# Kernel tuning notes

Hardware: AMD Instinct MI355X
Metric: run time of the kernel (lower is better)

Reference implementation:

```python
import jax, jax.numpy as jnp
import numpy as np


def setup_inputs() -> dict:
    key = jax.random.key(0)
    ks = jax.random.split(key, 11)
    B, S, D, H, O = 128, 512, 256, 512, 256
    sc = lambda fan_in: 1.0 / np.sqrt(fan_in)
    return {
        "inputs": jax.random.normal(ks[0], (B, S, D), dtype=jnp.float32),
        "time_diffs": jax.random.uniform(ks[1], (B, S), dtype=jnp.float32),
        "seq_lens": jax.random.randint(ks[2], (B,), 1, S, dtype=jnp.int32),
        "W_all": jax.random.normal(ks[3], (D, 4 * H), dtype=jnp.float32) * sc(D),
        "b_all": jax.random.normal(ks[4], (4 * H,), dtype=jnp.float32) * sc(D),
        "U_all": jax.random.normal(ks[5], (H, 4 * H), dtype=jnp.float32) * sc(H),
        "b_u": jax.random.normal(ks[6], (4 * H,), dtype=jnp.float32) * sc(H),
        "W_d": jax.random.normal(ks[7], (H, H), dtype=jnp.float32) * sc(H),
        "b_d": jax.random.normal(ks[8], (H,), dtype=jnp.float32) * sc(H),
        "W_out": jax.random.normal(ks[9], (H, O), dtype=jnp.float32) * sc(H),
        "b_out": jax.random.normal(ks[10], (O,), dtype=jnp.float32) * sc(H),
    }


def reference(inputs, time_diffs, seq_lens, W_all, b_all, U_all, b_u, W_d, b_d, W_out, b_out):
    B, S, D = inputs.shape
    H = W_d.shape[0]
    # Precompute input projection for all timesteps as one batched GEMM: [B,S,4H]
    Wx = jnp.einsum("bsd,dh->bsh", inputs, W_all) + b_all

    def step(carry, xs):
        h, c = carry
        wx, t = xs  # wx: [B,4H], t: [B]
        # time-decay adjustment of cell state
        c_st = jax.nn.sigmoid(c @ W_d + b_d)
        c_adj = c - c_st + c_st * t[:, None]
        outs = wx + h @ U_all + b_u
        f, i, o, g = jnp.split(outs, 4, axis=1)
        c_t = jax.nn.sigmoid(f) * c_adj + jax.nn.sigmoid(i) * jnp.tanh(g)
        h_t = jax.nn.sigmoid(o) * jnp.tanh(c_t)
        return (h_t, c_t), (h_t, c_t)

    h0 = jnp.zeros((B, H), dtype=inputs.dtype)
    c0 = jnp.zeros((B, H), dtype=inputs.dtype)
    # scan over time (leading axis)
    xs = (jnp.swapaxes(Wx, 0, 1), time_diffs.T)  # [S,B,4H], [S,B]
    _, (hs, cs) = jax.lax.scan(step, (h0, c0), xs)
    hs = jnp.swapaxes(hs, 0, 1)  # [B,S,H]
    cs = jnp.swapaxes(cs, 0, 1)
    outputs = jnp.einsum("bsh,ho->bso", hs, W_out) + b_out
    return outputs, hs, cs
```

## Files before the change

### kernel.cpp

```cpp
#include <hip/hip_runtime.h>

typedef __attribute__((ext_vector_type(8))) short short8;
typedef __attribute__((ext_vector_type(4))) float floatx4;
typedef unsigned short u16;
typedef __attribute__((ext_vector_type(4))) unsigned short u16x4;

#define B_ 128
#define S_ 512
#define D_ 256
#define H_ 512
#define O_ 256

__device__ __forceinline__ u16 f2bf(float f) {
  union { float f; unsigned u; } v; v.f = f;
  unsigned r = v.u + 0x7fffu + ((v.u >> 16) & 1u);
  return (u16)(r >> 16);
}
__device__ __forceinline__ float sigf(float x) { return 1.f / (1.f + __expf(-x)); }
__device__ __forceinline__ float tanhf_fast(float x) { return 1.f - 2.f / (__expf(2.f * x) + 1.f); }

__device__ __forceinline__ unsigned long long ld_u64_agent(const unsigned long long* p) {
  return __hip_atomic_load(p, __ATOMIC_RELAXED, __HIP_MEMORY_SCOPE_AGENT);
}

__global__ __launch_bounds__(256) void cvt_bf16_vec(const float* __restrict__ in,
                                                    u16* __restrict__ out, int n4) {
  int i = blockIdx.x * 256 + threadIdx.x;
  if (i < n4) {
    const float4 v = ((const float4*)in)[i];
    u16x4 o;
    o.x = f2bf(v.x); o.y = f2bf(v.y); o.z = f2bf(v.z); o.w = f2bf(v.w);
    ((u16x4*)out)[i] = o;
  }
}

__global__ __launch_bounds__(256) void transpose_cvt(const float* __restrict__ in,
                                                     u16* __restrict__ out, int R, int C) {
  int idx = blockIdx.x * 256 + threadIdx.x;
  if (idx < R * C) {
    int r = idx % R, c = idx / R;
    out[idx] = f2bf(in[(size_t)r * C + c]);
  }
}

#define PU 520
#define PX 264
#define SCAN_SMEM ((size_t)(4*16*PU + 4*16*PX + 3*16*PU) * 2 + (size_t)5*272*4)

__global__ __launch_bounds__(320, 1) void tlstm_scan(
    const u16* __restrict__ xbf,
    const float* __restrict__ tdiff,
    const u16* __restrict__ UallT,
    const u16* __restrict__ WallT,
    const u16* __restrict__ WdT,
    const float* __restrict__ b_all, const float* __restrict__ b_u,
    const float* __restrict__ b_d,
    u16* __restrict__ h_state,
    u16* __restrict__ c_state,
    unsigned* __restrict__ bar,
    float* __restrict__ d_hs, float* __restrict__ d_cs,
    u16* __restrict__ hs_bf)
{
  extern __shared__ char smem[];
  u16* ldsU  = (u16*)smem;
  u16* ldsX  = ldsU + 4 * 16 * PU;
  u16* ldsC  = ldsX + 4 * 16 * PX;
  u16* ldsH  = ldsC + 16 * PU;
  u16* ldsC2 = ldsH + 16 * PU;
  float* ldsP = (float*)(ldsC2 + 16 * PU);

  const int g = blockIdx.x & 7, mem = blockIdx.x >> 3;
  const int B0 = g * 16, U0 = mem * 16;
  const int tid = threadIdx.x;

  for (int i = tid; i < 4 * 16 * 64; i += 320) {
    int w = i >> 10, r = i & 1023, n = r >> 6, kb = r & 63;
    *(short8*)(ldsU + (w * 16 + n) * PU + kb * 8) =
        *(const short8*)(UallT + (size_t)(w * 512 + U0 + n) * 512 + kb * 8);
  }
  for (int i = tid; i < 4 * 16 * 32; i += 320) {
    int w = i >> 9, r = i & 511, n = r >> 5, kb = r & 31;
    *(short8*)(ldsX + (w * 16 + n) * PX + kb * 8) =
        *(const short8*)(WallT + (size_t)(w * 512 + U0 + n) * 256 + kb * 8);
  }
  for (int i = tid; i < 16 * 64; i += 320) {
    int n = i >> 6, kb = i & 63;
    *(short8*)(ldsC + n * PU + kb * 8) =
        *(const short8*)(WdT + (size_t)(U0 + n) * 512 + kb * 8);
  }

  const int em = tid >> 4, eu = tid & 15;
  const int ug = U0 + eu;
  const int ebb = B0 + em;
  float bf_ = 0.f, bi_ = 0.f, bo_ = 0.f, bg_ = 0.f, bd_ = 0.f;
  if (tid < 256) {
    bf_ = b_all[ug] + b_u[ug];
    bi_ = b_all[512 + ug] + b_u[512 + ug];
    bo_ = b_all[1024 + ug] + b_u[1024 + ug];
    bg_ = b_all[1536 + ug] + b_u[1536 + ug];
    bd_ = b_d[ug];
  }
  const int wv = tid >> 6, lane = tid & 63, lm = lane & 15, quad = lane >> 4;
  float creg = 0.f;

  short8 pxa[8];
  if (wv < 4) {
    const u16* xrow = xbf + ((size_t)(B0 + lm) * S_ + 0) * D_ + quad * 8;
#pragma unroll
    for (int it = 0; it < 8; ++it) pxa[it] = *(const short8*)(xrow + it * 32);
  }
  __syncthreads();

  for (int s = 0; s < S_; ++s) {
    const u16* hcur = h_state + (size_t)(s & 1) * B_ * H_;
    const u16* ccur = c_state + (size_t)(s & 1) * B_ * H_;
    u16* hnxt = h_state + (size_t)((s + 1) & 1) * B_ * H_;
    u16* cnxt = c_state + (size_t)((s + 1) & 1) * B_ * H_;

    unsigned long long hq[16];
    if (tid < 256) {
      const unsigned long long* hsrc = (const unsigned long long*)hcur + (size_t)B0 * 128;
      const unsigned long long* csrc = (const unsigned long long*)ccur + (size_t)B0 * 128;
#pragma unroll
      for (int k = 0; k < 16; ++k) {
        const int qq = tid + 256 * (k & 7);
        hq[k] = ld_u64_agent(((k < 8) ? hsrc : csrc) + qq);
      }
    }

    floatx4 accx = {0.f, 0.f, 0.f, 0.f};
    if (wv < 4) {
      const u16* bX = ldsX + (wv * 16 + lm) * PX + quad * 8;
#pragma unroll
      for (int it = 0; it < 8; ++it)
        accx = __builtin_amdgcn_mfma_f32_16x16x32_bf16(pxa[it], *(const short8*)(bX + it * 32), accx, 0, 0, 0);
    }

    if (tid < 256) {
#pragma unroll
      for (int k = 0; k < 16; ++k) {
        const int qq = tid + 256 * (k & 7);
        const int row = qq >> 7, c8 = qq & 127;
        *(unsigned long long*)(((k < 8) ? ldsH : ldsC2) + row * PU + c8 * 4) = hq[k];
      }
    }
    __syncthreads();

    floatx4 a0 = {0.f, 0.f, 0.f, 0.f}, a1 = {0.f, 0.f, 0.f, 0.f};
    if (wv < 4) {
      const u16* arow = ldsH + lm * PU + quad * 8;
      const u16* bU = ldsU + (wv * 16 + lm) * PU + quad * 8;
#pragma unroll
      for (int it = 0; it < 8; ++it) {
        a0 = __builtin_amdgcn_mfma_f32_16x16x32_bf16(*(const short8*)(arow + it * 32),
                                                     *(const short8*)(bU + it * 32), a0, 0, 0, 0);
        a1 = __builtin_amdgcn_mfma_f32_16x16x32_bf16(*(const short8*)(arow + (it + 8) * 32),
                                                     *(const short8*)(bU + (it + 8) * 32), a1, 0, 0, 0);
      }
    } else {
      const u16* arow = ldsC2 + lm * PU + quad * 8;
      const u16* bC = ldsC + lm * PU + quad * 8;
#pragma unroll
      for (int it = 0; it < 8; ++it) {
        a0 = __builtin_amdgcn_mfma_f32_16x16x32_bf16(*(const short8*)(arow + it * 32),
                                                     *(const short8*)(bC + it * 32), a0, 0, 0, 0);
        a1 = __builtin_amdgcn_mfma_f32_16x16x32_bf16(*(const short8*)(arow + (it + 8) * 32),
                                                     *(const short8*)(bC + (it + 8) * 32), a1, 0, 0, 0);
      }
    }
    {
      float* P = ldsP + wv * 272;
#pragma unroll
      for (int r = 0; r < 4; ++r)
        P[(quad * 4 + r) * 17 + lm] = accx[r] + a0[r] + a1[r];
    }
    __syncthreads();

    if (tid < 256) {
      const float f   = ldsP[0 * 272 + em * 17 + eu];
      const float ii  = ldsP[1 * 272 + em * 17 + eu];
      const float oo  = ldsP[2 * 272 + em * 17 + eu];
      const float ggv = ldsP[3 * 272 + em * 17 + eu];
      const float csp = ldsP[4 * 272 + em * 17 + eu];
      const float tt = tdiff[(size_t)ebb * S_ + s];
      const float cst = sigf(csp + bd_);
      const float cadj = creg - cst + cst * tt;
      const float fv = sigf(f + bf_), iv = sigf(ii + bi_), ov = sigf(oo + bo_);
      const float gv = tanhf_fast(ggv + bg_);
      const float ct = fv * cadj + iv * gv;
      const float ht = ov * tanhf_fast(ct);
      creg = ct;
      const size_t oidx = ((size_t)ebb * S_ + s) * H_ + ug;
      d_hs[oidx] = ht;
      d_cs[oidx] = ct;
      const unsigned hb = (unsigned)f2bf(ht);
      const unsigned cb = (unsigned)f2bf(ct);
      hs_bf[oidx] = (u16)hb;
      const unsigned hn = (unsigned)__shfl_xor((int)hb, 1);
      const unsigned cn = (unsigned)__shfl_xor((int)cb, 1);
      if (!(eu & 1)) {
        const size_t wi = ((size_t)ebb * H_ + ug) >> 1;
        __hip_atomic_store((unsigned*)hnxt + wi, hb | (hn << 16),
                           __ATOMIC_RELAXED, __HIP_MEMORY_SCOPE_AGENT);
        __hip_atomic_store((unsigned*)cnxt + wi, cb | (cn << 16),
                           __ATOMIC_RELAXED, __HIP_MEMORY_SCOPE_AGENT);
      }
    }

    if (wv < 4) {
      const int sn = (s + 1 < S_) ? s + 1 : s;
      const u16* xrow = xbf + ((size_t)(B0 + lm) * S_ + sn) * D_ + quad * 8;
#pragma unroll
      for (int it = 0; it < 8; ++it) pxa[it] = *(const short8*)(xrow + it * 32);
    }

    __syncthreads();
    if (tid == 0) {
      __hip_atomic_fetch_add(&bar[g * 64], 1u, __ATOMIC_RELAXED, __HIP_MEMORY_SCOPE_AGENT);
      const unsigned tgt = 32u * (unsigned)(s + 1);
      while (__hip_atomic_load(&bar[g * 64], __ATOMIC_RELAXED, __HIP_MEMORY_SCOPE_AGENT) < tgt)
        __builtin_amdgcn_s_sleep(2);
    }
    __syncthreads();
  }
}

__global__ __launch_bounds__(256, 4) void gemm2(const u16* __restrict__ A,
                                                const u16* __restrict__ Bt,
                                                const float* __restrict__ bias,
                                                float* __restrict__ C) {
  const int K = 512, N = 256;
  const int wave = threadIdx.x >> 6, lane = threadIdx.x & 63;
  const int wm = wave >> 1, wn = wave & 1;
  const int lm = lane & 15, quad = lane >> 4;
  const int Mb = blockIdx.x * 64 + wm * 32;
  const int Nb = blockIdx.y * 64 + wn * 32;
  const u16* a0 = A + (size_t)(Mb + lm) * K + quad * 8;
  const u16* a1 = a0 + (size_t)16 * K;
  const u16* b0 = Bt + (size_t)(Nb + lm) * K + quad * 8;
  const u16* b1 = b0 + (size_t)16 * K;
  floatx4 acc00 = {0,0,0,0}, acc01 = {0,0,0,0}, acc10 = {0,0,0,0}, acc11 = {0,0,0,0};
#pragma unroll 4
  for (int k = 0; k < K; k += 32) {
    short8 av0 = *(const short8*)(a0 + k);
    short8 av1 = *(const short8*)(a1 + k);
    short8 bv0 = *(const short8*)(b0 + k);
    short8 bv1 = *(const short8*)(b1 + k);
    acc00 = __builtin_amdgcn_mfma_f32_16x16x32_bf16(av0, bv0, acc00, 0, 0, 0);
    acc01 = __builtin_amdgcn_mfma_f32_16x16x32_bf16(av0, bv1, acc01, 0, 0, 0);
    acc10 = __builtin_amdgcn_mfma_f32_16x16x32_bf16(av1, bv0, acc10, 0, 0, 0);
    acc11 = __builtin_amdgcn_mfma_f32_16x16x32_bf16(av1, bv1, acc11, 0, 0, 0);
  }
  const float bia0 = bias[Nb + lm], bia1 = bias[Nb + 16 + lm];
#pragma unroll
  for (int r = 0; r < 4; ++r) {
    const int row0 = Mb + quad * 4 + r;
    C[(size_t)row0 * N + Nb + lm]            = acc00[r] + bia0;
    C[(size_t)row0 * N + Nb + 16 + lm]       = acc01[r] + bia1;
    C[(size_t)(row0 + 16) * N + Nb + lm]     = acc10[r] + bia0;
    C[(size_t)(row0 + 16) * N + Nb + 16 + lm] = acc11[r] + bia1;
  }
}

extern "C" void kernel_launch(void* const* d_in, const int* in_sizes, int n_in,
                              void* d_out, int out_size, void* d_ws, size_t ws_size,
                              hipStream_t stream) {
  const float* inputs = (const float*)d_in[0];
  const float* tdiff  = (const float*)d_in[1];
  const float* W_all = (const float*)d_in[3];
  const float* b_all = (const float*)d_in[4];
  const float* U_all = (const float*)d_in[5];
  const float* b_u   = (const float*)d_in[6];
  const float* W_d   = (const float*)d_in[7];
  const float* b_d   = (const float*)d_in[8];
  const float* W_out = (const float*)d_in[9];
  const float* b_out = (const float*)d_in[10];

  float* out = (float*)d_out;
  float* d_outputs = out;
  float* d_hs = out + (size_t)B_ * S_ * O_;
  float* d_cs = d_hs + (size_t)B_ * S_ * H_;

  char* ws = (char*)d_ws;
  size_t off = 0;
  auto alloc = [&](size_t bytes) {
    char* p = ws + off;
    off += (bytes + 255) & ~(size_t)255;
    return p;
  };
  u16* xbf      = (u16*)alloc((size_t)B_ * S_ * D_ * 2);
  u16* hs_bf    = (u16*)alloc((size_t)B_ * S_ * H_ * 2);
  u16* UallT    = (u16*)alloc((size_t)2048 * 512 * 2);
  u16* WallT    = (u16*)alloc((size_t)2048 * 256 * 2);
  u16* WdT      = (u16*)alloc((size_t)512 * 512 * 2);
  u16* WoutT    = (u16*)alloc((size_t)256 * 512 * 2);
  u16* h_state  = (u16*)alloc((size_t)2 * B_ * H_ * 2);
  u16* c_state  = (u16*)alloc((size_t)2 * B_ * H_ * 2);
  unsigned* bar = (unsigned*)alloc(4096);

  hipMemsetAsync(h_state, 0, (size_t)2 * B_ * H_ * 2, stream);
  hipMemsetAsync(c_state, 0, (size_t)2 * B_ * H_ * 2, stream);
  hipMemsetAsync(bar, 0, 4096, stream);

  cvt_bf16_vec<<<(B_ * S_ * D_ / 4 + 255) / 256, 256, 0, stream>>>(inputs, xbf, B_ * S_ * D_ / 4);
  transpose_cvt<<<(256 * 2048 + 255) / 256, 256, 0, stream>>>(W_all, WallT, 256, 2048);
  transpose_cvt<<<(512 * 2048 + 255) / 256, 256, 0, stream>>>(U_all, UallT, 512, 2048);
  transpose_cvt<<<(512 * 512 + 255) / 256, 256, 0, stream>>>(W_d, WdT, 512, 512);
  transpose_cvt<<<(512 * 256 + 255) / 256, 256, 0, stream>>>(W_out, WoutT, 512, 256);

  (void)hipFuncSetAttribute((const void*)tlstm_scan,
                            hipFuncAttributeMaxDynamicSharedMemorySize, (int)SCAN_SMEM);
  tlstm_scan<<<256, 320, SCAN_SMEM, stream>>>(xbf, tdiff, UallT, WallT, WdT,
                                              b_all, b_u, b_d, h_state, c_state,
                                              bar, d_hs, d_cs, hs_bf);
  gemm2<<<dim3(B_ * S_ / 64, O_ / 64), 256, 0, stream>>>(hs_bf, WoutT, b_out, d_outputs);
}
```

Before: 2.295 ms.

## Replace per-step counter barrier with per-wave flags polled by whole wave

The scan previously ended each timestep with a __syncthreads, an atomic add by one thread to a group counter, a spin, and another __syncthreads. Now each producing wave waits for its h/c state stores to complete, then writes a per-wave step flag. At the start of the next step every wave polls all 128 flags of its batch group with one 64-bit load per lane and __all. The large hs/cs/hs_bf output stores are moved after the flag publish so they no longer delay the dependency signal. This shortens the cross-block critical path but relies on the flag buffer being large enough (128 entries per group) and zero-initialised.

```diff
diff --git a/kernel.cpp b/kernel.cpp
--- a/kernel.cpp
+++ b/kernel.cpp
@@ -4,6 +4,7 @@
 typedef __attribute__((ext_vector_type(4))) float floatx4;
 typedef unsigned short u16;
 typedef __attribute__((ext_vector_type(4))) unsigned short u16x4;
+typedef unsigned long long u64;
 
 #define B_ 128
 #define S_ 512
@@ -19,7 +20,7 @@
 __device__ __forceinline__ float sigf(float x) { return 1.f / (1.f + __expf(-x)); }
 __device__ __forceinline__ float tanhf_fast(float x) { return 1.f - 2.f / (__expf(2.f * x) + 1.f); }
 
-__device__ __forceinline__ unsigned long long ld_u64_agent(const unsigned long long* p) {
+__device__ __forceinline__ u64 ld_u64_agent(const u64* p) {
   return __hip_atomic_load(p, __ATOMIC_RELAXED, __HIP_MEMORY_SCOPE_AGENT);
 }
 
@@ -46,6 +47,8 @@
 #define PU 520
 #define PX 264
 #define SCAN_SMEM ((size_t)(4*16*PU + 4*16*PX + 3*16*PU) * 2 + (size_t)5*272*4)
+
+#define MFMA_BF16 __builtin_amdgcn_mfma_f32_16x16x32_bf16
 
 __global__ __launch_bounds__(320, 1) void tlstm_scan(
     const u16* __restrict__ xbf,
@@ -72,6 +75,7 @@
   const int g = blockIdx.x & 7, mem = blockIdx.x >> 3;
   const int B0 = g * 16, U0 = mem * 16;
   const int tid = threadIdx.x;
+  unsigned* flg = bar + (size_t)g * 128;
 
   for (int i = tid; i < 4 * 16 * 64; i += 320) {
     int w = i >> 10, r = i & 1023, n = r >> 6, kb = r & 63;
@@ -112,15 +116,24 @@
   __syncthreads();
 
   for (int s = 0; s < S_; ++s) {
+    if (s) {
+      const unsigned tgt = (unsigned)s;
+      const u64* fq = (const u64*)flg + lane;
+      while (true) {
+        const u64 q = ld_u64_agent(fq);
+        const bool mine = ((unsigned)q >= tgt) & ((unsigned)(q >> 32) >= tgt);
+        if (__all(mine)) break;
+        __builtin_amdgcn_s_sleep(1);
+      }
+    }
+
     const u16* hcur = h_state + (size_t)(s & 1) * B_ * H_;
     const u16* ccur = c_state + (size_t)(s & 1) * B_ * H_;
-    u16* hnxt = h_state + (size_t)((s + 1) & 1) * B_ * H_;
-    u16* cnxt = c_state + (size_t)((s + 1) & 1) * B_ * H_;
-
-    unsigned long long hq[16];
+
+    u64 hq[16];
     if (tid < 256) {
-      const unsigned long long* hsrc = (const unsigned long long*)hcur + (size_t)B0 * 128;
-      const unsigned long long* csrc = (const unsigned long long*)ccur + (size_t)B0 * 128;
+      const u64* hsrc = (const u64*)hcur + (size_t)B0 * 128;
+      const u64* csrc = (const u64*)ccur + (size_t)B0 * 128;
 #pragma unroll
       for (int k = 0; k < 16; ++k) {
         const int qq = tid + 256 * (k & 7);
@@ -133,7 +146,7 @@
       const u16* bX = ldsX + (wv * 16 + lm) * PX + quad * 8;
 #pragma unroll
       for (int it = 0; it < 8; ++it)
-        accx = __builtin_amdgcn_mfma_f32_16x16x32_bf16(pxa[it], *(const short8*)(bX + it * 32), accx, 0, 0, 0);
+        accx = MFMA_BF16(pxa[it], *(const short8*)(bX + it * 32), accx, 0, 0, 0);
     }
 
     if (tid < 256) {
@@ -141,7 +154,7 @@
       for (int k = 0; k < 16; ++k) {
         const int qq = tid + 256 * (k & 7);
         const int row = qq >> 7, c8 = qq & 127;
-        *(unsigned long long*)(((k < 8) ? ldsH : ldsC2) + row * PU + c8 * 4) = hq[k];
+        *(u64*)(((k < 8) ? ldsH : ldsC2) + row * PU + c8 * 4) = hq[k];
       }
     }
     __syncthreads();
@@ -152,20 +165,20 @@
       const u16* bU = ldsU + (wv * 16 + lm) * PU + quad * 8;
 #pragma unroll
       for (int it = 0; it < 8; ++it) {
-        a0 = __builtin_amdgcn_mfma_f32_16x16x32_bf16(*(const short8*)(arow + it * 32),
-                                                     *(const short8*)(bU + it * 32), a0, 0, 0, 0);
-        a1 = __builtin_amdgcn_mfma_f32_16x16x32_bf16(*(const short8*)(arow + (it + 8) * 32),
-                                                     *(const short8*)(bU + (it + 8) * 32), a1, 0, 0, 0);
+        a0 = MFMA_BF16(*(const short8*)(arow + it * 32),
+                       *(const short8*)(bU + it * 32), a0, 0, 0, 0);
+        a1 = MFMA_BF16(*(const short8*)(arow + (it + 8) * 32),
+                       *(const short8*)(bU + (it + 8) * 32), a1, 0, 0, 0);
       }
     } else {
       const u16* arow = ldsC2 + lm * PU + quad * 8;
       const u16* bC = ldsC + lm * PU + quad * 8;
 #pragma unroll
       for (int it = 0; it < 8; ++it) {
-        a0 = __builtin_amdgcn_mfma_f32_16x16x32_bf16(*(const short8*)(arow + it * 32),
-                                                     *(const short8*)(bC + it * 32), a0, 0, 0, 0);
-        a1 = __builtin_amdgcn_mfma_f32_16x16x32_bf16(*(const short8*)(arow + (it + 8) * 32),
-                                                     *(const short8*)(bC + (it + 8) * 32), a1, 0, 0, 0);
+        a0 = MFMA_BF16(*(const short8*)(arow + it * 32),
+                       *(const short8*)(bC + it * 32), a0, 0, 0, 0);
+        a1 = MFMA_BF16(*(const short8*)(arow + (it + 8) * 32),
+                       *(const short8*)(bC + (it + 8) * 32), a1, 0, 0, 0);
       }
     }
     {
@@ -190,21 +203,27 @@
       const float ct = fv * cadj + iv * gv;
       const float ht = ov * tanhf_fast(ct);
       creg = ct;
-      const size_t oidx = ((size_t)ebb * S_ + s) * H_ + ug;
-      d_hs[oidx] = ht;
-      d_cs[oidx] = ct;
       const unsigned hb = (unsigned)f2bf(ht);
       const unsigned cb = (unsigned)f2bf(ct);
-      hs_bf[oidx] = (u16)hb;
       const unsigned hn = (unsigned)__shfl_xor((int)hb, 1);
       const unsigned cn = (unsigned)__shfl_xor((int)cb, 1);
       if (!(eu & 1)) {
+        u16* hnxt = h_state + (size_t)((s + 1) & 1) * B_ * H_;
+        u16* cnxt = c_state + (size_t)((s + 1) & 1) * B_ * H_;
         const size_t wi = ((size_t)ebb * H_ + ug) >> 1;
         __hip_atomic_store((unsigned*)hnxt + wi, hb | (hn << 16),
                            __ATOMIC_RELAXED, __HIP_MEMORY_SCOPE_AGENT);
         __hip_atomic_store((unsigned*)cnxt + wi, cb | (cn << 16),
                            __ATOMIC_RELAXED, __HIP_MEMORY_SCOPE_AGENT);
       }
+      asm volatile("s_waitcnt vmcnt(0)" ::: "memory");
+      if (lane == 0)
+        __hip_atomic_store(flg + mem * 4 + wv, (unsigned)(s + 1),
+                           __ATOMIC_RELAXED, __HIP_MEMORY_SCOPE_AGENT);
+      const size_t oidx = ((size_t)ebb * S_ + s) * H_ + ug;
+      d_hs[oidx] = ht;
+      d_cs[oidx] = ct;
+      hs_bf[oidx] = (u16)hb;
     }
 
     if (wv < 4) {
@@ -213,15 +232,6 @@
 #pragma unroll
       for (int it = 0; it < 8; ++it) pxa[it] = *(const short8*)(xrow + it * 32);
     }
-
-    __syncthreads();
-    if (tid == 0) {
-      __hip_atomic_fetch_add(&bar[g * 64], 1u, __ATOMIC_RELAXED, __HIP_MEMORY_SCOPE_AGENT);
-      const unsigned tgt = 32u * (unsigned)(s + 1);
-      while (__hip_atomic_load(&bar[g * 64], __ATOMIC_RELAXED, __HIP_MEMORY_SCOPE_AGENT) < tgt)
-        __builtin_amdgcn_s_sleep(2);
-    }
-    __syncthreads();
   }
 }
 
@@ -246,10 +256,10 @@
     short8 av1 = *(const short8*)(a1 + k);
     short8 bv0 = *(const short8*)(b0 + k);
     short8 bv1 = *(const short8*)(b1 + k);
-    acc00 = __builtin_amdgcn_mfma_f32_16x16x32_bf16(av0, bv0, acc00, 0, 0, 0);
-    acc01 = __builtin_amdgcn_mfma_f32_16x16x32_bf16(av0, bv1, acc01, 0, 0, 0);
-    acc10 = __builtin_amdgcn_mfma_f32_16x16x32_bf16(av1, bv0, acc10, 0, 0, 0);
-    acc11 = __builtin_amdgcn_mfma_f32_16x16x32_bf16(av1, bv1, acc11, 0, 0, 0);
+    acc00 = MFMA_BF16(av0, bv0, acc00, 0, 0, 0);
+    acc01 = MFMA_BF16(av0, bv1, acc01, 0, 0, 0);
+    acc10 = MFMA_BF16(av1, bv0, acc10, 0, 0, 0);
+    acc11 = MFMA_BF16(av1, bv1, acc11, 0, 0, 0);
   }
   const float bia0 = bias[Nb + lm], bia1 = bias[Nb + 16 + lm];
 #pragma unroll
```

Measured after the change: 4.133 ms. 80.1% more time.
